# Kernel tuning notes

Measured on AMD Instinct MI355X. Metric: run time of the kernel, lower is better.

The kernel has to match this reference:

```python
import jax, jax.numpy as jnp
import numpy as np

B, N, V, H, Z = 2048, 32, 10, 256, 64


def setup_inputs() -> dict:
    key = jax.random.key(0)
    ks = jax.random.split(key, 14)
    # strictly upper-triangular random DAG adjacency (topological order = vertex index)
    p = jax.random.uniform(ks[0], (B, N, N))
    tri = jnp.triu(jnp.ones((N, N), jnp.float32), k=1)
    adj = (p < 0.12).astype(jnp.float32) * tri
    node_types = jax.random.randint(ks[1], (B, N), 0, V).astype(jnp.int32)
    s = 0.05
    return dict(
        adj=adj,
        node_types=node_types,
        w_ih=jax.random.normal(ks[2], (V, 3 * H), jnp.float32) * s,
        w_hh=jax.random.normal(ks[3], (H, 3 * H), jnp.float32) * s,
        b_ih=jax.random.normal(ks[4], (3 * H,), jnp.float32) * s,
        b_hh=jax.random.normal(ks[5], (3 * H,), jnp.float32) * s,
        w_gate=jax.random.normal(ks[6], (H, H), jnp.float32) * s,
        b_gate=jax.random.normal(ks[7], (H,), jnp.float32) * s,
        w_map=jax.random.normal(ks[8], (H, H), jnp.float32) * s,
        w_mu=jax.random.normal(ks[9], (H, Z), jnp.float32) * s,
        b_mu=jax.random.normal(ks[10], (Z,), jnp.float32) * s,
        w_std=jax.random.normal(ks[11], (H, Z), jnp.float32) * s,
        b_std=jax.random.normal(ks[12], (Z,), jnp.float32) * s,
    )


def _gru_cell(x, h, w_ih, w_hh, b_ih, b_hh):
    # torch GRUCell math; weights stored [in, 3H]
    gi = x @ w_ih + b_ih  # [B, 3H]
    gh = h @ w_hh + b_hh
    i_r, i_z, i_n = jnp.split(gi, 3, axis=-1)
    h_r, h_z, h_n = jnp.split(gh, 3, axis=-1)
    r = jax.nn.sigmoid(i_r + h_r)
    z = jax.nn.sigmoid(i_z + h_z)
    n = jnp.tanh(i_n + r * h_n)
    return (1.0 - z) * n + z * h


def reference(adj, node_types, w_ih, w_hh, b_ih, b_hh, w_gate, b_gate, w_map,
              w_mu, b_mu, w_std, b_std):
    x_all = jax.nn.one_hot(node_types, V, dtype=adj.dtype)  # [B, N, V]
    hidden0 = jnp.zeros((B, N, H), adj.dtype)
    adj_cols = jnp.transpose(adj, (2, 0, 1))  # [N, B, N]; col v = predecessor mask of v
    x_seq = jnp.transpose(x_all, (1, 0, 2))   # [N, B, V]

    def step(hidden, inps):
        col, x, v = inps
        # gate(h_pred) * map(h_pred), summed over predecessors. map has no bias,
        # so non-predecessor (zero-masked) rows contribute exactly zero, matching
        # the padded-gather formulation in the original code.
        gm = jax.nn.sigmoid(hidden @ w_gate + b_gate) * (hidden @ w_map)  # [B, N, H]
        agg = jnp.einsum('bn,bnh->bh', col, gm)  # [B, H]; zero for v=0 (no preds)
        h_new = _gru_cell(x, agg, w_ih, w_hh, b_ih, b_hh)  # [B, H]
        hidden = jax.lax.dynamic_update_slice(hidden, h_new[:, None, :], (0, v, 0))
        return hidden, None

    hidden, _ = jax.lax.scan(step, hidden0, (adj_cols, x_seq, jnp.arange(N)))
    hg = hidden[:, -1, :]  # graph state = last vertex hidden
    mu = hg @ w_mu + b_mu
    sigma = hg @ w_std + b_std
    return (mu, sigma)
```

## Files before the change

### kernel.cpp

```cpp
#include <hip/hip_runtime.h>


#define BB 2048
#define NN 32
#define VV 10
#define HH 256
#define ZZ 64
#define BT 8
#define KC 8
#define NT1 48
#define NT2 32
#define WHH_ELEMS (NT1 * KC * 64 * 8)
#define WGM_ELEMS (NT2 * KC * 64 * 8)
#define GM_BYTE_OFF ((WHH_ELEMS + WGM_ELEMS) * 2)
#define SLAB_ELEMS (BT * NN * HH)
#define SLAB_BYTES (SLAB_ELEMS * 2)

typedef __attribute__((ext_vector_type(8))) short frag8;
typedef __attribute__((ext_vector_type(4))) float facc4;
typedef __attribute__((ext_vector_type(4))) unsigned short us4;
typedef __attribute__((ext_vector_type(8))) unsigned short us8;

__device__ __forceinline__ float bf2f(unsigned short u) {
    unsigned int x = ((unsigned int)u) << 16;
    return __builtin_bit_cast(float, x);
}
__device__ __forceinline__ unsigned short f2bf(float f) {
    unsigned int x = __builtin_bit_cast(unsigned int, f);
    x += 0x7FFFu + ((x >> 16) & 1u);
    return (unsigned short)(x >> 16);
}
__device__ __forceinline__ float sigm(float x) { return 1.0f / (1.0f + __expf(-x)); }
__device__ __forceinline__ float ldv(const float* p, size_t i) { return p[i]; }
__device__ __forceinline__ float ldv(const unsigned short* p, size_t i) { return bf2f(p[i]); }
__device__ __forceinline__ void stv(float* p, size_t i, float v) { p[i] = v; }
__device__ __forceinline__ void stv(unsigned short* p, size_t i, float v) { p[i] = f2bf(v); }
__device__ __forceinline__ us4 ntld4(const unsigned short* p) {
    return __builtin_nontemporal_load((const us4*)p);
}
__device__ __forceinline__ void ntst16(unsigned short* p, us8 v) {
    __builtin_nontemporal_store(v, (us8*)p);
}

__global__ void detect_dtype(const unsigned short* __restrict__ w, int* flag) {
    __shared__ int zc, bc;
    if (threadIdx.x == 0) { zc = 0; bc = 0; }
    __syncthreads();
    int z = 0, b = 0;
    for (int i = threadIdx.x; i < 2048; i += 256) {
        unsigned short lo = w[2 * i];
        if (lo == 0) z++;
        unsigned e = (lo >> 7) & 0xFFu;
        if (e >= 0x86u) b++;
    }
    atomicAdd(&zc, z); atomicAdd(&bc, b);
    __syncthreads();
    if (threadIdx.x == 0) *flag = (bc > 0 || zc > 512) ? 1 : 0;
}

template <typename T>
__global__ void repack_weights(const T* __restrict__ w_hh,
                               const T* __restrict__ w_gate,
                               const T* __restrict__ w_map,
                               unsigned short* __restrict__ whh_p,
                               unsigned short* __restrict__ wgm_p,
                               const int* __restrict__ flag, int want) {
    if (*flag != want) return;
    int t = blockIdx.x * blockDim.x + threadIdx.x;
    int lane = t & 63;
    int frag = t >> 6;
    int kbase = (lane >> 4) * 8;
    if (frag < NT1 * KC) {
        int jt = frag / KC, kc = frag % KC;
        int col = jt * 16 + (lane & 15);
        unsigned short* dst = whh_p + ((size_t)frag * 64 + lane) * 8;
        #pragma unroll
        for (int j = 0; j < 8; ++j)
            dst[j] = f2bf(ldv(w_hh, (size_t)(kc * 32 + kbase + j) * 768 + col));
    } else if (frag < (NT1 + NT2) * KC) {
        int f2 = frag - NT1 * KC;
        int jt = f2 / KC, kc = f2 % KC;
        int col = jt * 16 + (lane & 15);
        unsigned short* dst = wgm_p + ((size_t)f2 * 64 + lane) * 8;
        #pragma unroll
        for (int j = 0; j < 8; ++j) {
            int k = kc * 32 + kbase + j;
            dst[j] = f2bf((col < HH) ? ldv(w_gate, (size_t)k * HH + col)
                                     : ldv(w_map, (size_t)k * HH + (col - HH)));
        }
    }
}

template <typename T>
__global__ __launch_bounds__(1024, 4) void vae_main(
    const T* __restrict__ adj,
    const int* __restrict__ ntypes,
    const T* __restrict__ w_ih,
    const T* __restrict__ b_ih,
    const T* __restrict__ b_hh,
    const T* __restrict__ b_gate,
    const T* __restrict__ w_mu,
    const T* __restrict__ b_mu,
    const T* __restrict__ w_std,
    const T* __restrict__ b_std,
    const unsigned short* __restrict__ whh_p,
    const unsigned short* __restrict__ wgm_p,
    unsigned short* __restrict__ gm_base,
    T* __restrict__ out,
    int b_start,
    const int* __restrict__ flag, int want)
{
    if (*flag != want) return;

    __shared__ __align__(16) float agg[BT][HH];
    __shared__ __align__(16) unsigned short aggbf[16][264];
    __shared__ __align__(16) unsigned short hnew[16][264];
    __shared__ __align__(16) unsigned short gmrow[BT][HH];
    __shared__ unsigned int  amask[BT][NN];
    __shared__ int           ntva[BT][NN];
    __shared__ __align__(16) unsigned short wihL[VV * 776];
    __shared__ __align__(16) float bihL[768], bhhL[768], bgL[HH];

    const int tid  = threadIdx.x;
    const int lane = tid & 63;
    const int w    = tid >> 6;
    const int b0   = b_start + blockIdx.x * BT;

    unsigned short* gms = gm_base + (size_t)blockIdx.x * SLAB_ELEMS;

    const frag8* whh8 = (const frag8*)whh_p;
    const frag8* wgm8 = (const frag8*)wgm_p;

    for (int i = 8 * 264 + tid; i < 16 * 264; i += 1024) {
        ((unsigned short*)aggbf)[i] = 0;
        ((unsigned short*)hnew)[i]  = 0;
    }
    if (tid < 256) {
        int bi = tid >> 5, vv = tid & 31;
        unsigned m = 0;
        for (int n = 0; n < NN; ++n)
            if (ldv(adj, ((size_t)(b0 + bi) * NN + n) * NN + vv) != 0.0f) m |= (1u << n);
        amask[bi][vv] = m;
    } else if (tid < 512) {
        int idx = tid - 256;
        int bi = idx >> 5, vv = idx & 31;
        ntva[bi][vv] = ntypes[(b0 + bi) * NN + vv];
    }
    for (int i = tid; i < VV * 768; i += 1024) {
        int r = i / 768, c = i - r * 768;
        wihL[r * 776 + c] = f2bf(ldv(w_ih, (size_t)i));
    }
    for (int i = tid; i < 768; i += 1024) { bihL[i] = ldv(b_ih, i); bhhL[i] = ldv(b_hh, i); }
    if (tid < HH) bgL[tid] = ldv(b_gate, tid);

    frag8 wG[KC];
    {
        const frag8* pG = wgm8 + (size_t)w * (KC * 64) + lane;
        #pragma unroll
        for (int kc = 0; kc < KC; ++kc) wG[kc] = pG[kc * 64];
    }
    __syncthreads();

    for (int v = 0; v < NN; ++v) {
        if (w < BT) {
            const int bi = w;
            const int h4 = lane * 4;
            unsigned m0 = amask[bi][v];
            unsigned m  = (v > 0) ? (m0 & ~(1u << (v - 1))) : m0;
            float a0 = 0.f, a1 = 0.f, a2 = 0.f, a3 = 0.f;
            const unsigned short* rb = gms + (size_t)bi * NN * HH + h4;
            while (m) {
                int n = __builtin_ctz(m); m &= m - 1;
                us4 g = ntld4(rb + (size_t)n * HH);
                a0 += bf2f(g.x); a1 += bf2f(g.y); a2 += bf2f(g.z); a3 += bf2f(g.w);
            }
            if (v > 0 && ((m0 >> (v - 1)) & 1u)) {
                const unsigned short* gr = &gmrow[bi][h4];
                a0 += bf2f(gr[0]); a1 += bf2f(gr[1]);
                a2 += bf2f(gr[2]); a3 += bf2f(gr[3]);
            }
            *(float4*)&agg[bi][h4] = make_float4(a0, a1, a2, a3);
            ushort4 ab; ab.x = f2bf(a0); ab.y = f2bf(a1); ab.z = f2bf(a2); ab.w = f2bf(a3);
            *(ushort4*)&aggbf[bi][h4] = ab;
        } else if (w < 12 && v > 0) {
            const int bi = (w - 8) * 2 + (lane >> 5);
            const int c8 = (lane & 31) * 8;
            us8 val = *(const us8*)&gmrow[bi][c8];
            ntst16(gms + ((size_t)bi * NN + (v - 1)) * HH + c8, val);
        }
        __syncthreads();

        {
            frag8 afrag[KC];
            #pragma unroll
            for (int kc = 0; kc < KC; ++kc)
                afrag[kc] = *(const frag8*)&aggbf[lane & 15][kc * 32 + (lane >> 4) * 8];

            const int t = w;
            facc4 aR = {0.f, 0.f, 0.f, 0.f};
            facc4 aZ = {0.f, 0.f, 0.f, 0.f};
            facc4 aN = {0.f, 0.f, 0.f, 0.f};
            const frag8* pR = whh8 + (size_t)(t     ) * (KC * 64) + lane;
            const frag8* pZ = whh8 + (size_t)(t + 16) * (KC * 64) + lane;
            const frag8* pN = whh8 + (size_t)(t + 32) * (KC * 64) + lane;
            #pragma unroll
            for (int kc = 0; kc < KC; ++kc) {
                aR = __builtin_amdgcn_mfma_f32_16x16x32_bf16(afrag[kc], pR[kc * 64], aR, 0, 0, 0);
                aZ = __builtin_amdgcn_mfma_f32_16x16x32_bf16(afrag[kc], pZ[kc * 64], aZ, 0, 0, 0);
                aN = __builtin_amdgcn_mfma_f32_16x16x32_bf16(afrag[kc], pN[kc * 64], aN, 0, 0, 0);
            }
            const int col = t * 16 + (lane & 15);
            const int q = lane >> 4;
            if (q < 2) {
                const float bir  = bihL[col],       bhr = bhhL[col];
                const float biz  = bihL[col + 256], bhz = bhhL[col + 256];
                const float bin_ = bihL[col + 512], bhn = bhhL[col + 512];
                #pragma unroll
                for (int i = 0; i < 4; ++i) {
                    const int bi = 4 * q + i;
                    const int ty = ntva[bi][v] * 776;
                    const float xr = bf2f(wihL[ty + col]);
                    const float xz = bf2f(wihL[ty + col + 256]);
                    const float xn = bf2f(wihL[ty + col + 512]);
                    const float r = sigm(xr + bir + aR[i] + bhr);
                    const float z = sigm(xz + biz + aZ[i] + bhz);
                    const float n = tanhf(xn + bin_ + r * (aN[i] + bhn));
                    const float h = (1.f - z) * n + z * agg[bi][col];
                    hnew[bi][col] = f2bf(h);
                }
            }
        }
        __syncthreads();

        {
            frag8 hfrag[KC];
            #pragma unroll
            for (int kc = 0; kc < KC; ++kc)
                hfrag[kc] = *(const frag8*)&hnew[lane & 15][kc * 32 + (lane >> 4) * 8];

            const int t = w;
            facc4 aG = {0.f, 0.f, 0.f, 0.f};
            facc4 aM = {0.f, 0.f, 0.f, 0.f};
            const frag8* pM = wgm8 + (size_t)(t + 16) * (KC * 64) + lane;
            #pragma unroll
            for (int kc = 0; kc < KC; ++kc) {
                aG = __builtin_amdgcn_mfma_f32_16x16x32_bf16(hfrag[kc], wG[kc], aG, 0, 0, 0);
                aM = __builtin_amdgcn_mfma_f32_16x16x32_bf16(hfrag[kc], pM[kc * 64], aM, 0, 0, 0);
            }
            const int col = t * 16 + (lane & 15);
            const int q = lane >> 4;
            if (q < 2) {
                const float bg = bgL[col];
                #pragma unroll
                for (int i = 0; i < 4; ++i) {
                    const int bi = 4 * q + i;
                    gmrow[bi][col] = f2bf(sigm(aG[i] + bg) * aM[i]);
                }
            }
        }
        __syncthreads();
    }

    {
        const int bi = w >> 1, half = w & 1, z = lane;
        float am = 0.f, as = 0.f;
        const int h0 = half * 128;
        #pragma unroll 4
        for (int h = h0; h < h0 + 128; ++h) {
            const float hv = bf2f(hnew[bi][h]);
            am += hv * ldv(w_mu, (size_t)h * ZZ + z);
            as += hv * ldv(w_std, (size_t)h * ZZ + z);
        }
        agg[bi][half * 64 + z]       = am;
        agg[bi][128 + half * 64 + z] = as;
    }
    __syncthreads();
    if (w < BT) {
        const int bi = w, z = lane;
        const float am = agg[bi][z] + agg[bi][64 + z] + ldv(b_mu, z);
        const float as = agg[bi][128 + z] + agg[bi][192 + z] + ldv(b_std, z);
        stv(out, (size_t)(b0 + bi) * ZZ + z, am);
        stv(out, (size_t)BB * ZZ + (size_t)(b0 + bi) * ZZ + z, as);
    }
}

extern "C" void kernel_launch(void* const* d_in, const int* in_sizes, int n_in,
                              void* d_out, int out_size, void* d_ws, size_t ws_size,
                              hipStream_t stream)
{
    unsigned short* whh_p = (unsigned short*)d_ws;
    unsigned short* wgm_p = whh_p + WHH_ELEMS;
    unsigned short* gm_base = wgm_p + WGM_ELEMS;

    size_t flag_off = (ws_size >= 8) ? ((ws_size - 4) & ~(size_t)3) : 0;
    int* flag = (int*)((char*)d_ws + flag_off);

    long long avail = (long long)flag_off - (long long)GM_BYTE_OFF;
    int cb = (int)(avail / SLAB_BYTES);
    if (cb < 1) cb = 1;
    if (cb > BB / BT) cb = BB / BT;

    detect_dtype<<<dim3(1), 256, 0, stream>>>((const unsigned short*)d_in[2], flag);

    repack_weights<float><<<dim3(160), 256, 0, stream>>>(
        (const float*)d_in[3], (const float*)d_in[6], (const float*)d_in[8],
        whh_p, wgm_p, flag, 1);
    repack_weights<unsigned short><<<dim3(160), 256, 0, stream>>>(
        (const unsigned short*)d_in[3], (const unsigned short*)d_in[6],
        (const unsigned short*)d_in[8], whh_p, wgm_p, flag, 0);

    const int nblk = BB / BT;
    for (int blk0 = 0; blk0 < nblk; blk0 += cb) {
        int g = nblk - blk0; if (g > cb) g = cb;
        vae_main<float><<<dim3(g), 1024, 0, stream>>>(
            (const float*)d_in[0], (const int*)d_in[1], (const float*)d_in[2],
            (const float*)d_in[4], (const float*)d_in[5], (const float*)d_in[7],
            (const float*)d_in[9], (const float*)d_in[10], (const float*)d_in[11],
            (const float*)d_in[12],
            whh_p, wgm_p, gm_base, (float*)d_out, blk0 * BT, flag, 1);
        vae_main<unsigned short><<<dim3(g), 1024, 0, stream>>>(
            (const unsigned short*)d_in[0], (const int*)d_in[1],
            (const unsigned short*)d_in[2], (const unsigned short*)d_in[4],
            (const unsigned short*)d_in[5], (const unsigned short*)d_in[7],
            (const unsigned short*)d_in[9], (const unsigned short*)d_in[10],
            (const unsigned short*)d_in[11], (const unsigned short*)d_in[12],
            whh_p, wgm_p, gm_base, (unsigned short*)d_out, blk0 * BT, flag, 0);
    }
}
```

Baseline: 562.5 us.

## Keep per-vertex gate*map history in LDS instead of global workspace slabs

Stores the full gate*map history for each block's 8 graphs (8x32x256 bf16, 128KB) in shared memory, replacing the global-memory slab that was written each step and read back for the predecessor sums. This removes the global round-trip and the chunked multi-launch loop, so a single launch covers the whole batch. It also folds b_ih into a precomputed fp32 w_ih table in the repack kernel, keeps the map weight fragments in registers, and reuses the padding rows of aggbf/hnew for the fp32 agg buffers. The large LDS footprint caps residency at about one 1024-thread block per CU.

```diff
diff --git a/kernel.cpp b/kernel.cpp
--- a/kernel.cpp
+++ b/kernel.cpp
@@ -12,14 +12,10 @@
 #define NT2 32
 #define WHH_ELEMS (NT1 * KC * 64 * 8)
 #define WGM_ELEMS (NT2 * KC * 64 * 8)
-#define GM_BYTE_OFF ((WHH_ELEMS + WGM_ELEMS) * 2)
-#define SLAB_ELEMS (BT * NN * HH)
-#define SLAB_BYTES (SLAB_ELEMS * 2)
 
 typedef __attribute__((ext_vector_type(8))) short frag8;
 typedef __attribute__((ext_vector_type(4))) float facc4;
 typedef __attribute__((ext_vector_type(4))) unsigned short us4;
-typedef __attribute__((ext_vector_type(8))) unsigned short us8;
 
 __device__ __forceinline__ float bf2f(unsigned short u) {
     unsigned int x = ((unsigned int)u) << 16;
@@ -35,12 +31,6 @@
 __device__ __forceinline__ float ldv(const unsigned short* p, size_t i) { return bf2f(p[i]); }
 __device__ __forceinline__ void stv(float* p, size_t i, float v) { p[i] = v; }
 __device__ __forceinline__ void stv(unsigned short* p, size_t i, float v) { p[i] = f2bf(v); }
-__device__ __forceinline__ us4 ntld4(const unsigned short* p) {
-    return __builtin_nontemporal_load((const us4*)p);
-}
-__device__ __forceinline__ void ntst16(unsigned short* p, us8 v) {
-    __builtin_nontemporal_store(v, (us8*)p);
-}
 
 __global__ void detect_dtype(const unsigned short* __restrict__ w, int* flag) {
     __shared__ int zc, bc;
@@ -62,8 +52,11 @@
 __global__ void repack_weights(const T* __restrict__ w_hh,
                                const T* __restrict__ w_gate,
                                const T* __restrict__ w_map,
+                               const T* __restrict__ w_ih,
+                               const T* __restrict__ b_ih,
                                unsigned short* __restrict__ whh_p,
                                unsigned short* __restrict__ wgm_p,
+                               float* __restrict__ wihG,
                                const int* __restrict__ flag, int want) {
     if (*flag != want) return;
     int t = blockIdx.x * blockDim.x + threadIdx.x;
@@ -88,6 +81,12 @@
             dst[j] = f2bf((col < HH) ? ldv(w_gate, (size_t)k * HH + col)
                                      : ldv(w_map, (size_t)k * HH + (col - HH)));
         }
+    } else {
+        int idx = t - (NT1 + NT2) * KC * 64;
+        if (idx < VV * 768) {
+            int c = idx % 768;
+            wihG[idx] = ldv(w_ih, (size_t)idx) + ldv(b_ih, (size_t)c);
+        }
     }
 }
 
@@ -95,8 +94,6 @@
 __global__ __launch_bounds__(1024, 4) void vae_main(
     const T* __restrict__ adj,
     const int* __restrict__ ntypes,
-    const T* __restrict__ w_ih,
-    const T* __restrict__ b_ih,
     const T* __restrict__ b_hh,
     const T* __restrict__ b_gate,
     const T* __restrict__ w_mu,
@@ -105,36 +102,31 @@
     const T* __restrict__ b_std,
     const unsigned short* __restrict__ whh_p,
     const unsigned short* __restrict__ wgm_p,
-    unsigned short* __restrict__ gm_base,
+    const float* __restrict__ wihG,
     T* __restrict__ out,
-    int b_start,
     const int* __restrict__ flag, int want)
 {
     if (*flag != want) return;
 
-    __shared__ __align__(16) float agg[BT][HH];
+    __shared__ __align__(16) unsigned short gmAll[BT][NN][HH];
     __shared__ __align__(16) unsigned short aggbf[16][264];
     __shared__ __align__(16) unsigned short hnew[16][264];
-    __shared__ __align__(16) unsigned short gmrow[BT][HH];
     __shared__ unsigned int  amask[BT][NN];
     __shared__ int           ntva[BT][NN];
-    __shared__ __align__(16) unsigned short wihL[VV * 776];
-    __shared__ __align__(16) float bihL[768], bhhL[768], bgL[HH];
+    __shared__ __align__(16) float bhhL[768];
+    __shared__ float bgL[HH];
+
+    float* const aggA = (float*)&aggbf[8][0];
+    float* const aggB = (float*)&hnew[8][0];
 
     const int tid  = threadIdx.x;
     const int lane = tid & 63;
     const int w    = tid >> 6;
-    const int b0   = b_start + blockIdx.x * BT;
-
-    unsigned short* gms = gm_base + (size_t)blockIdx.x * SLAB_ELEMS;
+    const int b0   = blockIdx.x * BT;
 
     const frag8* whh8 = (const frag8*)whh_p;
     const frag8* wgm8 = (const frag8*)wgm_p;
 
-    for (int i = 8 * 264 + tid; i < 16 * 264; i += 1024) {
-        ((unsigned short*)aggbf)[i] = 0;
-        ((unsigned short*)hnew)[i]  = 0;
-    }
     if (tid < 256) {
         int bi = tid >> 5, vv = tid & 31;
         unsigned m = 0;
@@ -146,18 +138,15 @@
         int bi = idx >> 5, vv = idx & 31;
         ntva[bi][vv] = ntypes[(b0 + bi) * NN + vv];
     }
-    for (int i = tid; i < VV * 768; i += 1024) {
-        int r = i / 768, c = i - r * 768;
-        wihL[r * 776 + c] = f2bf(ldv(w_ih, (size_t)i));
-    }
-    for (int i = tid; i < 768; i += 1024) { bihL[i] = ldv(b_ih, i); bhhL[i] = ldv(b_hh, i); }
+    for (int i = tid; i < 768; i += 1024) bhhL[i] = ldv(b_hh, i);
     if (tid < HH) bgL[tid] = ldv(b_gate, tid);
 
-    frag8 wG[KC];
+    frag8 wG[KC], wM[KC];
     {
         const frag8* pG = wgm8 + (size_t)w * (KC * 64) + lane;
+        const frag8* pM = wgm8 + (size_t)(w + 16) * (KC * 64) + lane;
         #pragma unroll
-        for (int kc = 0; kc < KC; ++kc) wG[kc] = pG[kc * 64];
+        for (int kc = 0; kc < KC; ++kc) { wG[kc] = pG[kc * 64]; wM[kc] = pM[kc * 64]; }
     }
     __syncthreads();
 
@@ -165,38 +154,48 @@
         if (w < BT) {
             const int bi = w;
             const int h4 = lane * 4;
-            unsigned m0 = amask[bi][v];
-            unsigned m  = (v > 0) ? (m0 & ~(1u << (v - 1))) : m0;
+            unsigned m = amask[bi][v];
             float a0 = 0.f, a1 = 0.f, a2 = 0.f, a3 = 0.f;
-            const unsigned short* rb = gms + (size_t)bi * NN * HH + h4;
+            const unsigned short* rb = &gmAll[bi][0][0] + h4;
             while (m) {
-                int n = __builtin_ctz(m); m &= m - 1;
-                us4 g = ntld4(rb + (size_t)n * HH);
-                a0 += bf2f(g.x); a1 += bf2f(g.y); a2 += bf2f(g.z); a3 += bf2f(g.w);
-            }
-            if (v > 0 && ((m0 >> (v - 1)) & 1u)) {
-                const unsigned short* gr = &gmrow[bi][h4];
-                a0 += bf2f(gr[0]); a1 += bf2f(gr[1]);
-                a2 += bf2f(gr[2]); a3 += bf2f(gr[3]);
-            }
-            *(float4*)&agg[bi][h4] = make_float4(a0, a1, a2, a3);
+                const int n0 = __builtin_ctz(m); m &= m - 1;
+                const us4 g0 = *(const us4*)(rb + n0 * HH);
+                if (m) {
+                    const int n1 = __builtin_ctz(m); m &= m - 1;
+                    const us4 g1 = *(const us4*)(rb + n1 * HH);
+                    a0 += bf2f(g0.x) + bf2f(g1.x);
+                    a1 += bf2f(g0.y) + bf2f(g1.y);
+                    a2 += bf2f(g0.z) + bf2f(g1.z);
+                    a3 += bf2f(g0.w) + bf2f(g1.w);
+                } else {
+                    a0 += bf2f(g0.x); a1 += bf2f(g0.y);
+                    a2 += bf2f(g0.z); a3 += bf2f(g0.w);
+                }
+            }
+            float* ap = (bi < 4) ? (aggA + bi * 256) : (aggB + (bi - 4) * 256);
+            *(float4*)(ap + h4) = make_float4(a0, a1, a2, a3);
             ushort4 ab; ab.x = f2bf(a0); ab.y = f2bf(a1); ab.z = f2bf(a2); ab.w = f2bf(a3);
             *(ushort4*)&aggbf[bi][h4] = ab;
-        } else if (w < 12 && v > 0) {
-            const int bi = (w - 8) * 2 + (lane >> 5);
-            const int c8 = (lane & 31) * 8;
-            us8 val = *(const us8*)&gmrow[bi][c8];
-            ntst16(gms + ((size_t)bi * NN + (v - 1)) * HH + c8, val);
         }
         __syncthreads();
 
         {
+            const int t = w;
+            const int col = t * 16 + (lane & 15);
+            const int q = lane >> 4;
+            float xr[4], xz[4], xn[4];
+            if (q < 2) {
+                #pragma unroll
+                for (int i = 0; i < 4; ++i) {
+                    const float* wr = wihG + (size_t)ntva[4 * q + i][v] * 768 + col;
+                    xr[i] = wr[0]; xz[i] = wr[256]; xn[i] = wr[512];
+                }
+            }
             frag8 afrag[KC];
             #pragma unroll
             for (int kc = 0; kc < KC; ++kc)
                 afrag[kc] = *(const frag8*)&aggbf[lane & 15][kc * 32 + (lane >> 4) * 8];
 
-            const int t = w;
             facc4 aR = {0.f, 0.f, 0.f, 0.f};
             facc4 aZ = {0.f, 0.f, 0.f, 0.f};
             facc4 aN = {0.f, 0.f, 0.f, 0.f};
@@ -209,24 +208,15 @@
                 aZ = __builtin_amdgcn_mfma_f32_16x16x32_bf16(afrag[kc], pZ[kc * 64], aZ, 0, 0, 0);
                 aN = __builtin_amdgcn_mfma_f32_16x16x32_bf16(afrag[kc], pN[kc * 64], aN, 0, 0, 0);
             }
-            const int col = t * 16 + (lane & 15);
-            const int q = lane >> 4;
             if (q < 2) {
-                const float bir  = bihL[col],       bhr = bhhL[col];
-                const float biz  = bihL[col + 256], bhz = bhhL[col + 256];
-                const float bin_ = bihL[col + 512], bhn = bhhL[col + 512];
+                const float bhr = bhhL[col], bhz = bhhL[col + 256], bhn = bhhL[col + 512];
+                const float* ap = (q == 0) ? aggA : aggB;
                 #pragma unroll
                 for (int i = 0; i < 4; ++i) {
-                    const int bi = 4 * q + i;
-                    const int ty = ntva[bi][v] * 776;
-                    const float xr = bf2f(wihL[ty + col]);
-                    const float xz = bf2f(wihL[ty + col + 256]);
-                    const float xn = bf2f(wihL[ty + col + 512]);
-                    const float r = sigm(xr + bir + aR[i] + bhr);
-                    const float z = sigm(xz + biz + aZ[i] + bhz);
-                    const float n = tanhf(xn + bin_ + r * (aN[i] + bhn));
-                    const float h = (1.f - z) * n + z * agg[bi][col];
-                    hnew[bi][col] = f2bf(h);
+                    const float r = sigm(xr[i] + aR[i] + bhr);
+                    const float z = sigm(xz[i] + aZ[i] + bhz);
+                    const float n = tanhf(xn[i] + r * (aN[i] + bhn));
+                    hnew[4 * q + i][col] = f2bf((1.f - z) * n + z * ap[i * 256 + col]);
                 }
             }
         }
@@ -238,24 +228,20 @@
             for (int kc = 0; kc < KC; ++kc)
                 hfrag[kc] = *(const frag8*)&hnew[lane & 15][kc * 32 + (lane >> 4) * 8];
 
-            const int t = w;
             facc4 aG = {0.f, 0.f, 0.f, 0.f};
             facc4 aM = {0.f, 0.f, 0.f, 0.f};
-            const frag8* pM = wgm8 + (size_t)(t + 16) * (KC * 64) + lane;
             #pragma unroll
             for (int kc = 0; kc < KC; ++kc) {
                 aG = __builtin_amdgcn_mfma_f32_16x16x32_bf16(hfrag[kc], wG[kc], aG, 0, 0, 0);
-                aM = __builtin_amdgcn_mfma_f32_16x16x32_bf16(hfrag[kc], pM[kc * 64], aM, 0, 0, 0);
-            }
-            const int col = t * 16 + (lane & 15);
+                aM = __builtin_amdgcn_mfma_f32_16x16x32_bf16(hfrag[kc], wM[kc], aM, 0, 0, 0);
+            }
+            const int col = w * 16 + (lane & 15);
             const int q = lane >> 4;
             if (q < 2) {
                 const float bg = bgL[col];
                 #pragma unroll
-                for (int i = 0; i < 4; ++i) {
-                    const int bi = 4 * q + i;
-                    gmrow[bi][col] = f2bf(sigm(aG[i] + bg) * aM[i]);
-                }
+                for (int i = 0; i < 4; ++i)
+                    gmAll[4 * q + i][v][col] = f2bf(sigm(aG[i] + bg) * aM[i]);
             }
         }
         __syncthreads();
@@ -271,14 +257,16 @@
             am += hv * ldv(w_mu, (size_t)h * ZZ + z);
             as += hv * ldv(w_std, (size_t)h * ZZ + z);
         }
-        agg[bi][half * 64 + z]       = am;
-        agg[bi][128 + half * 64 + z] = as;
+        float* sc = (bi < 4) ? (aggA + bi * 256) : (aggB + (bi - 4) * 256);
+        sc[half * 64 + z]       = am;
+        sc[128 + half * 64 + z] = as;
     }
     __syncthreads();
     if (w < BT) {
         const int bi = w, z = lane;
-        const float am = agg[bi][z] + agg[bi][64 + z] + ldv(b_mu, z);
-        const float as = agg[bi][128 + z] + agg[bi][192 + z] + ldv(b_std, z);
+        const float* sc = (bi < 4) ? (aggA + bi * 256) : (aggB + (bi - 4) * 256);
+        const float am = sc[z] + sc[64 + z] + ldv(b_mu, z);
+        const float as = sc[128 + z] + sc[192 + z] + ldv(b_std, z);
         stv(out, (size_t)(b0 + bi) * ZZ + z, am);
         stv(out, (size_t)BB * ZZ + (size_t)(b0 + bi) * ZZ + z, as);
     }
@@ -290,40 +278,33 @@
 {
     unsigned short* whh_p = (unsigned short*)d_ws;
     unsigned short* wgm_p = whh_p + WHH_ELEMS;
-    unsigned short* gm_base = wgm_p + WGM_ELEMS;
+    float* wihG = (float*)(wgm_p + WGM_ELEMS);
 
     size_t flag_off = (ws_size >= 8) ? ((ws_size - 4) & ~(size_t)3) : 0;
     int* flag = (int*)((char*)d_ws + flag_off);
 
-    long long avail = (long long)flag_off - (long long)GM_BYTE_OFF;
-    int cb = (int)(avail / SLAB_BYTES);
-    if (cb < 1) cb = 1;
-    if (cb > BB / BT) cb = BB / BT;
-
     detect_dtype<<<dim3(1), 256, 0, stream>>>((const unsigned short*)d_in[2], flag);
 
-    repack_weights<float><<<dim3(160), 256, 0, stream>>>(
+    repack_weights<float><<<dim3(190), 256, 0, stream>>>(
         (const float*)d_in[3], (const float*)d_in[6], (const float*)d_in[8],
-        whh_p, wgm_p, flag, 1);
-    repack_weights<unsigned short><<<dim3(160), 256, 0, stream>>>(
+        (const float*)d_in[2], (const float*)d_in[4],
+        whh_p, wgm_p, wihG, flag, 1);
+    repack_weights<unsigned short><<<dim3(190), 256, 0, stream>>>(
         (const unsigned short*)d_in[3], (const unsigned short*)d_in[6],
-        (const unsigned short*)d_in[8], whh_p, wgm_p, flag, 0);
-
-    const int nblk = BB / BT;
-    for (int blk0 = 0; blk0 < nblk; blk0 += cb) {
-        int g = nblk - blk0; if (g > cb) g = cb;
-        vae_main<float><<<dim3(g), 1024, 0, stream>>>(
-            (const float*)d_in[0], (const int*)d_in[1], (const float*)d_in[2],
-            (const float*)d_in[4], (const float*)d_in[5], (const float*)d_in[7],
-            (const float*)d_in[9], (const float*)d_in[10], (const float*)d_in[11],
-            (const float*)d_in[12],
-            whh_p, wgm_p, gm_base, (float*)d_out, blk0 * BT, flag, 1);
-        vae_main<unsigned short><<<dim3(g), 1024, 0, stream>>>(
-            (const unsigned short*)d_in[0], (const int*)d_in[1],
-            (const unsigned short*)d_in[2], (const unsigned short*)d_in[4],
-            (const unsigned short*)d_in[5], (const unsigned short*)d_in[7],
-            (const unsigned short*)d_in[9], (const unsigned short*)d_in[10],
-            (const unsigned short*)d_in[11], (const unsigned short*)d_in[12],
-            whh_p, wgm_p, gm_base, (unsigned short*)d_out, blk0 * BT, flag, 0);
-    }
-}
+        (const unsigned short*)d_in[8], (const unsigned short*)d_in[2],
+        (const unsigned short*)d_in[4],
+        whh_p, wgm_p, wihG, flag, 0);
+
+    vae_main<float><<<dim3(BB / BT), 1024, 0, stream>>>(
+        (const float*)d_in[0], (const int*)d_in[1],
+        (const float*)d_in[5], (const float*)d_in[7],
+        (const float*)d_in[9], (const float*)d_in[10],
+        (const float*)d_in[11], (const float*)d_in[12],
+        whh_p, wgm_p, wihG, (float*)d_out, flag, 1);
+    vae_main<unsigned short><<<dim3(BB / BT), 1024, 0, stream>>>(
+        (const unsigned short*)d_in[0], (const int*)d_in[1],
+        (const unsigned short*)d_in[5], (const unsigned short*)d_in[7],
+        (const unsigned short*)d_in[9], (const unsigned short*)d_in[10],
+        (const unsigned short*)d_in[11], (const unsigned short*)d_in[12],
+        whh_p, wgm_p, wihG, (unsigned short*)d_out, flag, 0);
+}
```

Result: faster. 541.9 us (-3.7%).
